# Optimization experiments

Hardware: AMD Instinct MI355X
Metric: run time of the kernel (lower is better)

The kernel has to match this reference:

```python
import jax, jax.numpy as jnp
import numpy as np

B, S, D, H = 2, 2048, 1024, 16
HD = D // H  # 64


def setup_inputs() -> dict:
    key = jax.random.key(0)
    k1, k2, k3, k4, k5, k6 = jax.random.split(key, 6)
    x = jax.random.normal(k1, (B, S, D), dtype=jnp.float32)
    # binary mask source (1.0 = masked-out position), multiplied by -1e9 inside
    mask = (jax.random.uniform(k2, (B, S, S), dtype=jnp.float32) < 0.1).astype(jnp.float32)
    lim = 1.0 / np.sqrt(D)
    Wqkv = jax.random.uniform(k3, (D, 3 * D), dtype=jnp.float32, minval=-lim, maxval=lim)
    bqkv = jax.random.uniform(k4, (3 * D,), dtype=jnp.float32, minval=-lim, maxval=lim)
    Wo = jax.random.uniform(k5, (D, D), dtype=jnp.float32, minval=-lim, maxval=lim)
    bo = jax.random.uniform(k6, (D,), dtype=jnp.float32, minval=-lim, maxval=lim)
    return {"x": x, "mask": mask, "Wqkv": Wqkv, "bqkv": bqkv, "Wo": Wo, "bo": bo}


def reference(x, mask, Wqkv, bqkv, Wo, bo):
    b, s, d = x.shape
    qkv = x @ Wqkv + bqkv                              # [B,S,3D]
    qkv = qkv.reshape(b, s, 3, H, HD).transpose(2, 0, 3, 1, 4)  # [3,B,H,S,HD]
    q, k, v = qkv[0], qkv[1], qkv[2]
    scale = 1.0 / jnp.sqrt(jnp.float32(HD))
    scores = jnp.einsum('bhqd,bhkd->bhqk', q, k) * scale
    scores = scores + mask[:, None, :, :] * (-1e9)     # broadcast over heads
    attn = jax.nn.softmax(scores, axis=-1)             # [B,H,S,S]
    values = jnp.einsum('bhqk,bhkd->bhqd', attn, v)    # [B,H,S,HD]
    # faithful to source: permute(1,0,2,3) then reshape(B,S,H*HD)
    values = values.transpose(1, 0, 2, 3).reshape(b, s, H * HD)
    return values @ Wo + bo
```

## Files before the change

kernel.cpp:

```cpp
#include <hip/hip_runtime.h>
#include <stdint.h>

#define BB 2
#define SS 2048
#define DD 1024
#define HH 16
#define HD 64
#define BH 32
#define BS 4096

typedef short bf16x8 __attribute__((ext_vector_type(8)));
typedef float f32x4 __attribute__((ext_vector_type(4)));

static __device__ __forceinline__ unsigned short f2bf(float f) {
    union { float f; unsigned int u; } x;
    x.f = f;
    unsigned int u = x.u;
    unsigned int r = u + 0x7FFFu + ((u >> 16) & 1u);
    return (unsigned short)(r >> 16);
}

static __device__ __forceinline__ void gld16(unsigned short* lds, const unsigned short* g) {
    __builtin_amdgcn_global_load_lds(
        (const __attribute__((address_space(1))) unsigned int*)g,
        (__attribute__((address_space(3))) unsigned int*)lds,
        16, 0, 0);
}

__global__ __launch_bounds__(256) void prep(
    const float* __restrict__ x, unsigned short* __restrict__ xb,
    const float* __restrict__ Wqkv, unsigned short* __restrict__ WqkvT,
    const float* __restrict__ Wo, unsigned short* __restrict__ WoT,
    const float* __restrict__ mask, unsigned int* __restrict__ mbitsT) {
    __shared__ float tile[32][33];
    int bid = blockIdx.x;
    int tid = threadIdx.x;
    if (bid < 4096) {
        int i = (bid * 256 + tid) * 4;
        float4 v = *(const float4*)(x + i);
        ushort4 o;
        o.x = f2bf(v.x); o.y = f2bf(v.y); o.z = f2bf(v.z); o.w = f2bf(v.w);
        *(ushort4*)(xb + i) = o;
    } else if (bid < 8192) {
        const float* W;
        unsigned short* WT;
        int N, t;
        if (bid < 7168) { W = Wqkv; WT = WqkvT; N = 3072; t = bid - 4096; }
        else            { W = Wo;   WT = WoT;   N = 1024; t = bid - 7168; }
        const int K = 1024;
        int nx = N >> 5;
        int n0 = (t % nx) * 32, k0 = (t / nx) * 32;
        int tx = tid & 31, ty = tid >> 5;
#pragma unroll
        for (int i = 0; i < 4; i++)
            tile[ty + i * 8][tx] = W[(size_t)(k0 + ty + i * 8) * N + n0 + tx];
        __syncthreads();
#pragma unroll
        for (int i = 0; i < 4; i++)
            WT[(size_t)(n0 + ty + i * 8) * K + k0 + tx] = f2bf(tile[tx][ty + i * 8]);
    } else {
        size_t i = (size_t)(bid - 8192) * 256 + tid;
        float v = mask[i];
        unsigned long long bal = __ballot(v != 0.0f);
        int lane = tid & 63;
        int kw = (int)((i & 2047) >> 5);
        int sq = (int)((i >> 11) & 2047);
        int b = (int)(i >> 22);
        if (lane == 0)
            mbitsT[((size_t)b * 64 + kw) * 2048 + sq] = (unsigned int)bal;
        else if (lane == 32)
            mbitsT[((size_t)b * 64 + kw) * 2048 + sq] = (unsigned int)(bal >> 32);
    }
}

__global__ __launch_bounds__(256) void qkv_gemm(
    const unsigned short* __restrict__ xb,
    const unsigned short* __restrict__ WqkvT,
    const float* __restrict__ bqkv,
    unsigned short* __restrict__ q_ws,
    unsigned short* __restrict__ k_ws,
    unsigned short* __restrict__ vB) {
    __shared__ unsigned short ldsA[4096], ldsB[4096];
    int gx = blockIdx.x;
    int tid = threadIdx.x;
    int m0 = (gx / 24) * 128, n0 = (gx % 24) * 128;
    int w = tid >> 6, lane = tid & 63, quad = lane >> 4, l15 = lane & 15;

    int r = tid >> 2, p = tid & 3;
    int c = (p - (r >> 1)) & 3;
    const unsigned short* gA0 = xb + (size_t)(m0 + r) * 1024 + c * 8;
    const unsigned short* gA1 = gA0 + (size_t)64 * 1024;
    const unsigned short* gB0 = WqkvT + (size_t)(n0 + r) * 1024 + c * 8;
    const unsigned short* gB1 = gB0 + (size_t)64 * 1024;
    unsigned short* lA0 = ldsA + w * 512;
    unsigned short* lA1 = ldsA + 2048 + w * 512;
    unsigned short* lB0 = ldsB + w * 512;
    unsigned short* lB1 = ldsB + 2048 + w * 512;

    int wm = w >> 1, wn = w & 1;
    int posq = ((quad + (l15 >> 1)) & 3) * 8;
    int aoff = (wm * 64 + l15) * 32 + posq;
    int boff = (wn * 64 + l15) * 32 + posq;

    f32x4 acc[4][4] = {};
    for (int k0 = 0; k0 < 1024; k0 += 32) {
        __syncthreads();
        gld16(lA0, gA0 + k0);
        gld16(lA1, gA1 + k0);
        gld16(lB0, gB0 + k0);
        gld16(lB1, gB1 + k0);
        __syncthreads();
        bf16x8 af[4], bfr[4];
#pragma unroll
        for (int i = 0; i < 4; i++) {
            af[i]  = *(const bf16x8*)(ldsA + aoff + i * 512);
            bfr[i] = *(const bf16x8*)(ldsB + boff + i * 512);
        }
#pragma unroll
        for (int i = 0; i < 4; i++)
#pragma unroll
            for (int j = 0; j < 4; j++)
                acc[i][j] = __builtin_amdgcn_mfma_f32_16x16x32_bf16(af[i], bfr[j], acc[i][j], 0, 0, 0);
    }

    int t = n0 >> 10;
    int ncol0 = n0 + wn * 64;
    int hh = (ncol0 >> 6) & 15;
    int Rb = m0 + wm * 64 + quad * 4;

    if (t == 2) {
        int rowbase = m0 + wm * 64;
        int b = rowbase >> 11;
        int kt = (rowbase >> 6) & 31;
        int bh = b * 16 + hh;
#pragma unroll
        for (int j = 0; j < 4; j++) {
            int hd = j * 16 + l15;
            float bias = bqkv[ncol0 + hd];
#pragma unroll
            for (int i = 0; i < 4; i++) {
                unsigned short* dst = vB +
                    (((((size_t)bh * 32 + kt) * 2 + (i >> 1)) * 4 + quad) * 64 + hd) * 8 + (i & 1) * 4;
                ushort4 pk;
                pk.x = f2bf(acc[i][j][0] + bias);
                pk.y = f2bf(acc[i][j][1] + bias);
                pk.z = f2bf(acc[i][j][2] + bias);
                pk.w = f2bf(acc[i][j][3] + bias);
                *(ushort4*)dst = pk;
            }
        }
    } else {
        unsigned short* dst = (t == 0) ? q_ws : k_ws;
#pragma unroll
        for (int j = 0; j < 4; j++) {
            int hd = j * 16 + l15;
            float bias = bqkv[ncol0 + hd];
#pragma unroll
            for (int i = 0; i < 4; i++) {
                int row = Rb + i * 16;
                int b = row >> 11, s = row & 2047;
                int bh = b * 16 + hh;
#pragma unroll
                for (int rr = 0; rr < 4; rr++)
                    dst[((size_t)(bh * 2048 + s + rr)) * 64 + hd] = f2bf(acc[i][j][rr] + bias);
            }
        }
    }
}

__global__ __launch_bounds__(256) void out_gemm(
    const unsigned short* __restrict__ Amat,
    const unsigned short* __restrict__ WoT,
    const float* __restrict__ bo,
    float* __restrict__ out) {
    __shared__ unsigned short ldsA[4096], ldsB[2048];
    int gx = blockIdx.x;
    int m0 = (gx / 16) * 128, n0 = (gx % 16) * 64;
    int tid = threadIdx.x;
    int w = tid >> 6, lane = tid & 63, quad = lane >> 4, l15 = lane & 15;

    int r = tid >> 2, p = tid & 3;
    int c = (p - (r >> 1)) & 3;
    const unsigned short* gA0 = Amat + (size_t)(m0 + r) * 1024 + c * 8;
    const unsigned short* gA1 = gA0 + (size_t)64 * 1024;
    const unsigned short* gB0 = WoT + (size_t)(n0 + r) * 1024 + c * 8;
    unsigned short* lA0 = ldsA + w * 512;
    unsigned short* lA1 = ldsA + 2048 + w * 512;
    unsigned short* lB0 = ldsB + w * 512;

    int wm = w >> 1, wn = w & 1;
    int posq = ((quad + (l15 >> 1)) & 3) * 8;
    int aoff = (wm * 64 + l15) * 32 + posq;
    int boff = (wn * 32 + l15) * 32 + posq;

    f32x4 acc[4][2] = {};
    for (int k0 = 0; k0 < 1024; k0 += 32) {
        __syncthreads();
        gld16(lA0, gA0 + k0);
        gld16(lA1, gA1 + k0);
        gld16(lB0, gB0 + k0);
        __syncthreads();
        bf16x8 af[4], bfr[2];
#pragma unroll
        for (int i = 0; i < 4; i++) af[i] = *(const bf16x8*)(ldsA + aoff + i * 512);
#pragma unroll
        for (int j = 0; j < 2; j++) bfr[j] = *(const bf16x8*)(ldsB + boff + j * 512);
#pragma unroll
        for (int i = 0; i < 4; i++)
#pragma unroll
            for (int j = 0; j < 2; j++)
                acc[i][j] = __builtin_amdgcn_mfma_f32_16x16x32_bf16(af[i], bfr[j], acc[i][j], 0, 0, 0);
    }
    int ncol0 = n0 + wn * 32;
    int Rb = m0 + wm * 64 + quad * 4;
#pragma unroll
    for (int j = 0; j < 2; j++) {
        int col = ncol0 + j * 16 + l15;
        float bias = bo[col];
#pragma unroll
        for (int i = 0; i < 4; i++) {
            int row = Rb + i * 16;
#pragma unroll
            for (int rr = 0; rr < 4; rr++)
                out[(size_t)(row + rr) * 1024 + col] = acc[i][j][rr] + bias;
        }
    }
}

__global__ __launch_bounds__(256) void attn(
    const unsigned short* __restrict__ q_ws,
    const unsigned short* __restrict__ k_ws,
    const unsigned short* __restrict__ vB,
    const unsigned int* __restrict__ mbitsT,
    unsigned short* __restrict__ o_ws) {
    __shared__ unsigned short ldsK[4096];
    __shared__ unsigned short ldsV[4096];

    int tid = threadIdx.x;
    int w = tid >> 6, lane = tid & 63, quad = lane >> 4, l15 = lane & 15;
    int bx = blockIdx.x;
    int bh = bx >> 5, qt = bx & 31;
    int b = bh >> 4, h = bh & 15;

    int q = qt * 64 + w * 16 + l15;
    const unsigned short* qptr = q_ws + ((size_t)(bh * 2048 + q)) * 64 + quad * 8;
    bf16x8 qf0 = *(const bf16x8*)(qptr);
    bf16x8 qf1 = *(const bf16x8*)(qptr + 32);

    const float c2 = 0.125f * 1.44269504089f;
    const float Cs = c2 * 8388608.0f;
    const float Ds = (127.0f - 16.0f) * 8388608.0f;

    const unsigned int* mb = mbitsT + (size_t)b * 64 * 2048 + q;
    const unsigned short* kbase = k_ws + (size_t)bh * 2048 * 64;
    const unsigned short* vbb = vB + (size_t)bh * 32 * 4096;

    int srow = (lane >> 3);
    int spos = lane & 7;
    unsigned short* dK0 = ldsK + w * 1024 + lane * 8;
    unsigned short* dK1 = dK0 + 512;
    unsigned short* dV0 = ldsV + w * 1024 + lane * 8;
    unsigned short* dV1 = dV0 + 512;
    int r0 = w * 16 + srow;
    int r1 = r0 + 8;
    int g0 = spos ^ (r0 & 7);
    int g1 = spos ^ (r1 & 7);

    f32x4 oacc[4] = {};
    f32x4 lacc = {};
    bf16x8 onesA;
#pragma unroll
    for (int j = 0; j < 8; j++) onesA[j] = (short)0x3F80;

    int sw = (l15 & 7);
    int q4 = quad * 4;
    for (int kt = 0; kt < 32; kt++) {
        __syncthreads();
        gld16(dK0, kbase + ((size_t)(kt * 64 + r0)) * 64 + g0 * 8);
        gld16(dK1, kbase + ((size_t)(kt * 64 + r1)) * 64 + g1 * 8);
        {
            const unsigned short* vsrc = vbb + (size_t)kt * 4096 + w * 1024 + lane * 8;
            gld16(dV0, vsrc);
            gld16(dV1, vsrc + 512);
        }
        __syncthreads();

        f32x4 sacc[4];
#pragma unroll
        for (int nt = 0; nt < 4; nt++) {
            const unsigned short* kr = ldsK + (nt * 16 + l15) * 64;
            bf16x8 kf0, kf1;
            __builtin_memcpy(&kf0, kr + (quad ^ sw) * 8, 16);
            __builtin_memcpy(&kf1, kr + ((quad + 4) ^ sw) * 8, 16);
            f32x4 z = {};
            z = __builtin_amdgcn_mfma_f32_16x16x32_bf16(kf0, qf0, z, 0, 0, 0);
            z = __builtin_amdgcn_mfma_f32_16x16x32_bf16(kf1, qf1, z, 0, 0, 0);
            sacc[nt] = z;
        }
        unsigned int w0 = mb[(size_t)(2 * kt) * 2048];
        unsigned int w1 = mb[(size_t)(2 * kt + 1) * 2048];
        unsigned int s0 = w0 >> q4;
        unsigned int s1 = w1 >> q4;
        unsigned int dw[4][2];
#pragma unroll
        for (int nt = 0; nt < 4; nt++) {
            unsigned int sel = (nt & 2) ? s1 : s0;
            unsigned int u[4];
#pragma unroll
            for (int rr = 0; rr < 4; rr++) {
                float y = __builtin_fmaf(sacc[nt][rr], Cs, Ds);
                if ((sel >> ((nt & 1) * 16 + rr)) & 1u) y = 0.f;
                u[rr] = (unsigned int)(int)y;
            }
            dw[nt][0] = __builtin_amdgcn_perm(u[1], u[0], 0x07060302u);
            dw[nt][1] = __builtin_amdgcn_perm(u[3], u[2], 0x07060302u);
        }
#pragma unroll
        for (int ks2 = 0; ks2 < 2; ks2++) {
            union { bf16x8 v; unsigned int d[4]; } bfr;
            bfr.d[0] = dw[2 * ks2][0];
            bfr.d[1] = dw[2 * ks2][1];
            bfr.d[2] = dw[2 * ks2 + 1][0];
            bfr.d[3] = dw[2 * ks2 + 1][1];
#pragma unroll
            for (int nb = 0; nb < 4; nb++) {
                bf16x8 vf;
                __builtin_memcpy(&vf, ldsV + ((ks2 * 4 + quad) * 64 + nb * 16 + l15) * 8, 16);
                oacc[nb] = __builtin_amdgcn_mfma_f32_16x16x32_bf16(vf, bfr.v, oacc[nb], 0, 0, 0);
            }
            lacc = __builtin_amdgcn_mfma_f32_16x16x32_bf16(onesA, bfr.v, lacc, 0, 0, 0);
        }
    }

    float linv = 1.0f / lacc[0];
    unsigned short* base = o_ws + ((size_t)((h * 2 + b) * 2048 + q)) * 64;
#pragma unroll
    for (int nb = 0; nb < 4; nb++) {
        ushort4 pk;
        pk.x = f2bf(oacc[nb][0] * linv);
        pk.y = f2bf(oacc[nb][1] * linv);
        pk.z = f2bf(oacc[nb][2] * linv);
        pk.w = f2bf(oacc[nb][3] * linv);
        *(ushort4*)(base + nb * 16 + quad * 4) = pk;
    }
}


extern "C" void kernel_launch(void* const* d_in, const int* in_sizes, int n_in,
                              void* d_out, int out_size, void* d_ws, size_t ws_size,
                              hipStream_t stream) {
    const float* x    = (const float*)d_in[0];
    const float* mask = (const float*)d_in[1];
    const float* Wqkv = (const float*)d_in[2];
    const float* bqkv = (const float*)d_in[3];
    const float* Wo   = (const float*)d_in[4];
    const float* bo   = (const float*)d_in[5];
    float* out = (float*)d_out;

    char* ws = (char*)d_ws;
    unsigned short* xb    = (unsigned short*)(ws);
    unsigned short* WqkvT = (unsigned short*)(ws + ((size_t)8 << 20));
    unsigned short* WoT   = (unsigned short*)(ws + ((size_t)14 << 20));
    unsigned short* q_ws  = (unsigned short*)(ws + ((size_t)16 << 20));
    unsigned short* k_ws  = (unsigned short*)(ws + ((size_t)24 << 20));
    unsigned short* vB    = (unsigned short*)(ws + ((size_t)32 << 20));
    unsigned short* o_ws  = (unsigned short*)(ws + ((size_t)40 << 20));
    unsigned int*   mbits = (unsigned int*)(ws + ((size_t)48 << 20));

    prep<<<8192 + 32768, 256, 0, stream>>>(x, xb, Wqkv, WqkvT, Wo, WoT, mask, mbits);
    qkv_gemm<<<768, 256, 0, stream>>>(xb, WqkvT, bqkv, q_ws, k_ws, vB);
    attn<<<1024, 256, 0, stream>>>(q_ws, k_ws, vB, mbits, o_ws);
    out_gemm<<<512, 256, 0, stream>>>(o_ws, WoT, bo, out);
}
```

Measured before the change: 231.4 us.

## Double-buffer K/V tiles and mask words in attention, remap block order

The attention loop now uses two LDS buffers for K and V. The next tile's global-to-LDS loads and mask-word loads are issued before computing on the current tile, which replaces the two barriers per iteration with one. The goal is to hide global load latency behind the MFMA work. Block indices are also permuted so that consecutive workgroups land on different (b,h) groups, which may improve cache and XCD locality. LDS use doubles to 32KB per block, which could lower occupancy.

```diff
diff --git a/kernel.cpp b/kernel.cpp
--- a/kernel.cpp
+++ b/kernel.cpp
@@ -233,12 +233,13 @@
     const unsigned short* __restrict__ vB,
     const unsigned int* __restrict__ mbitsT,
     unsigned short* __restrict__ o_ws) {
-    __shared__ unsigned short ldsK[4096];
-    __shared__ unsigned short ldsV[4096];
+    __shared__ unsigned short ldsK[8192];
+    __shared__ unsigned short ldsV[8192];
 
     int tid = threadIdx.x;
     int w = tid >> 6, lane = tid & 63, quad = lane >> 4, l15 = lane & 15;
-    int bx = blockIdx.x;
+    int bxr = blockIdx.x;
+    int bx = ((bxr & 7) << 7) | (bxr >> 3);
     int bh = bx >> 5, qt = bx & 31;
     int b = bh >> 4, h = bh & 15;
 
@@ -258,13 +259,14 @@
     int srow = (lane >> 3);
     int spos = lane & 7;
     unsigned short* dK0 = ldsK + w * 1024 + lane * 8;
-    unsigned short* dK1 = dK0 + 512;
     unsigned short* dV0 = ldsV + w * 1024 + lane * 8;
-    unsigned short* dV1 = dV0 + 512;
     int r0 = w * 16 + srow;
     int r1 = r0 + 8;
     int g0 = spos ^ (r0 & 7);
     int g1 = spos ^ (r1 & 7);
+    const unsigned short* kS0 = kbase + (size_t)r0 * 64 + g0 * 8;
+    const unsigned short* kS1 = kbase + (size_t)r1 * 64 + g1 * 8;
+    const unsigned short* vS  = vbb + (size_t)w * 1024 + lane * 8;
 
     f32x4 oacc[4] = {};
     f32x4 lacc = {};
@@ -274,21 +276,39 @@
 
     int sw = (l15 & 7);
     int q4 = quad * 4;
+
+    gld16(dK0, kS0);
+    gld16(dK0 + 512, kS1);
+    gld16(dV0, vS);
+    gld16(dV0 + 512, vS + 512);
+    unsigned int mw0 = mb[0];
+    unsigned int mw1 = mb[2048];
+    __syncthreads();
+
     for (int kt = 0; kt < 32; kt++) {
-        __syncthreads();
-        gld16(dK0, kbase + ((size_t)(kt * 64 + r0)) * 64 + g0 * 8);
-        gld16(dK1, kbase + ((size_t)(kt * 64 + r1)) * 64 + g1 * 8);
-        {
-            const unsigned short* vsrc = vbb + (size_t)kt * 4096 + w * 1024 + lane * 8;
-            gld16(dV0, vsrc);
-            gld16(dV1, vsrc + 512);
-        }
-        __syncthreads();
+        int co = (kt & 1) << 12;
+
+        unsigned int nw0 = 0, nw1 = 0;
+        if (kt < 31) {
+            int so = co ^ 4096;
+            const unsigned short* kn = kS0 + (size_t)(kt + 1) * 4096;
+            const unsigned short* kn1 = kS1 + (size_t)(kt + 1) * 4096;
+            const unsigned short* vn = vS + (size_t)(kt + 1) * 4096;
+            gld16(dK0 + so, kn);
+            gld16(dK0 + so + 512, kn1);
+            gld16(dV0 + so, vn);
+            gld16(dV0 + so + 512, vn + 512);
+            nw0 = mb[(size_t)(2 * kt + 2) * 2048];
+            nw1 = mb[(size_t)(2 * kt + 3) * 2048];
+        }
+
+        const unsigned short* Kc = ldsK + co;
+        const unsigned short* Vc = ldsV + co;
 
         f32x4 sacc[4];
 #pragma unroll
         for (int nt = 0; nt < 4; nt++) {
-            const unsigned short* kr = ldsK + (nt * 16 + l15) * 64;
+            const unsigned short* kr = Kc + (nt * 16 + l15) * 64;
             bf16x8 kf0, kf1;
             __builtin_memcpy(&kf0, kr + (quad ^ sw) * 8, 16);
             __builtin_memcpy(&kf1, kr + ((quad + 4) ^ sw) * 8, 16);
@@ -297,10 +317,8 @@
             z = __builtin_amdgcn_mfma_f32_16x16x32_bf16(kf1, qf1, z, 0, 0, 0);
             sacc[nt] = z;
         }
-        unsigned int w0 = mb[(size_t)(2 * kt) * 2048];
-        unsigned int w1 = mb[(size_t)(2 * kt + 1) * 2048];
-        unsigned int s0 = w0 >> q4;
-        unsigned int s1 = w1 >> q4;
+        unsigned int s0 = mw0 >> q4;
+        unsigned int s1 = mw1 >> q4;
         unsigned int dw[4][2];
 #pragma unroll
         for (int nt = 0; nt < 4; nt++) {
@@ -325,11 +343,15 @@
 #pragma unroll
             for (int nb = 0; nb < 4; nb++) {
                 bf16x8 vf;
-                __builtin_memcpy(&vf, ldsV + ((ks2 * 4 + quad) * 64 + nb * 16 + l15) * 8, 16);
+                __builtin_memcpy(&vf, Vc + ((ks2 * 4 + quad) * 64 + nb * 16 + l15) * 8, 16);
                 oacc[nb] = __builtin_amdgcn_mfma_f32_16x16x32_bf16(vf, bfr.v, oacc[nb], 0, 0, 0);
             }
             lacc = __builtin_amdgcn_mfma_f32_16x16x32_bf16(onesA, bfr.v, lacc, 0, 0, 0);
         }
+
+        __syncthreads();
+        mw0 = nw0;
+        mw1 = nw1;
     }
 
     float linv = 1.0f / lacc[0];
```

New measurement: 234.7 us. Within noise of the previous version (+1.5%).

## Double-buffer K/V tiles in attention, prefetch mask, remap blocks, set wave priority

Applied to the files above, without the earlier changes.

The attention kernel now uses two LDS buffers for K and V. It issues the global-to-LDS loads for the next key tile, and the next mask words, before computing on the current tile, which cuts one barrier per iteration and overlaps load latency with MFMA work. The block index is also permuted so that neighbouring workgroups handle different heads, and s_setprio raises wave priority around the MFMA sections. The cost is double the LDS footprint, which may lower occupancy. Correctness now relies on the single trailing barrier ordering buffer reuse.

```diff
diff --git a/kernel.cpp b/kernel.cpp
--- a/kernel.cpp
+++ b/kernel.cpp
@@ -233,12 +233,13 @@
     const unsigned short* __restrict__ vB,
     const unsigned int* __restrict__ mbitsT,
     unsigned short* __restrict__ o_ws) {
-    __shared__ unsigned short ldsK[4096];
-    __shared__ unsigned short ldsV[4096];
+    __shared__ unsigned short ldsK[8192];
+    __shared__ unsigned short ldsV[8192];
 
     int tid = threadIdx.x;
     int w = tid >> 6, lane = tid & 63, quad = lane >> 4, l15 = lane & 15;
-    int bx = blockIdx.x;
+    int bxr = blockIdx.x;
+    int bx = ((bxr & 7) << 7) | (bxr >> 3);
     int bh = bx >> 5, qt = bx & 31;
     int b = bh >> 4, h = bh & 15;
 
@@ -258,13 +259,15 @@
     int srow = (lane >> 3);
     int spos = lane & 7;
     unsigned short* dK0 = ldsK + w * 1024 + lane * 8;
-    unsigned short* dK1 = dK0 + 512;
     unsigned short* dV0 = ldsV + w * 1024 + lane * 8;
-    unsigned short* dV1 = dV0 + 512;
     int r0 = w * 16 + srow;
     int r1 = r0 + 8;
     int g0 = spos ^ (r0 & 7);
     int g1 = spos ^ (r1 & 7);
+    const unsigned short* kS0n = kbase + (size_t)r0 * 64 + g0 * 8;
+    const unsigned short* kS1n = kbase + (size_t)r1 * 64 + g1 * 8;
+    const unsigned short* vSn  = vbb + (size_t)w * 1024 + lane * 8;
+    const unsigned int* mbn = mb;
 
     f32x4 oacc[4] = {};
     f32x4 lacc = {};
@@ -274,63 +277,89 @@
 
     int sw = (l15 & 7);
     int q4 = quad * 4;
-    for (int kt = 0; kt < 32; kt++) {
-        __syncthreads();
-        gld16(dK0, kbase + ((size_t)(kt * 64 + r0)) * 64 + g0 * 8);
-        gld16(dK1, kbase + ((size_t)(kt * 64 + r1)) * 64 + g1 * 8);
-        {
-            const unsigned short* vsrc = vbb + (size_t)kt * 4096 + w * 1024 + lane * 8;
-            gld16(dV0, vsrc);
-            gld16(dV1, vsrc + 512);
-        }
-        __syncthreads();
-
-        f32x4 sacc[4];
-#pragma unroll
-        for (int nt = 0; nt < 4; nt++) {
-            const unsigned short* kr = ldsK + (nt * 16 + l15) * 64;
-            bf16x8 kf0, kf1;
-            __builtin_memcpy(&kf0, kr + (quad ^ sw) * 8, 16);
-            __builtin_memcpy(&kf1, kr + ((quad + 4) ^ sw) * 8, 16);
-            f32x4 z = {};
-            z = __builtin_amdgcn_mfma_f32_16x16x32_bf16(kf0, qf0, z, 0, 0, 0);
-            z = __builtin_amdgcn_mfma_f32_16x16x32_bf16(kf1, qf1, z, 0, 0, 0);
-            sacc[nt] = z;
-        }
-        unsigned int w0 = mb[(size_t)(2 * kt) * 2048];
-        unsigned int w1 = mb[(size_t)(2 * kt + 1) * 2048];
-        unsigned int s0 = w0 >> q4;
-        unsigned int s1 = w1 >> q4;
-        unsigned int dw[4][2];
-#pragma unroll
-        for (int nt = 0; nt < 4; nt++) {
-            unsigned int sel = (nt & 2) ? s1 : s0;
-            unsigned int u[4];
-#pragma unroll
-            for (int rr = 0; rr < 4; rr++) {
-                float y = __builtin_fmaf(sacc[nt][rr], Cs, Ds);
-                if ((sel >> ((nt & 1) * 16 + rr)) & 1u) y = 0.f;
-                u[rr] = (unsigned int)(int)y;
-            }
-            dw[nt][0] = __builtin_amdgcn_perm(u[1], u[0], 0x07060302u);
-            dw[nt][1] = __builtin_amdgcn_perm(u[3], u[2], 0x07060302u);
-        }
-#pragma unroll
-        for (int ks2 = 0; ks2 < 2; ks2++) {
-            union { bf16x8 v; unsigned int d[4]; } bfr;
-            bfr.d[0] = dw[2 * ks2][0];
-            bfr.d[1] = dw[2 * ks2][1];
-            bfr.d[2] = dw[2 * ks2 + 1][0];
-            bfr.d[3] = dw[2 * ks2 + 1][1];
-#pragma unroll
-            for (int nb = 0; nb < 4; nb++) {
-                bf16x8 vf;
-                __builtin_memcpy(&vf, ldsV + ((ks2 * 4 + quad) * 64 + nb * 16 + l15) * 8, 16);
-                oacc[nb] = __builtin_amdgcn_mfma_f32_16x16x32_bf16(vf, bfr.v, oacc[nb], 0, 0, 0);
-            }
-            lacc = __builtin_amdgcn_mfma_f32_16x16x32_bf16(onesA, bfr.v, lacc, 0, 0, 0);
-        }
-    }
+
+    gld16(dK0, kS0n);
+    gld16(dK0 + 512, kS1n);
+    gld16(dV0, vSn);
+    gld16(dV0 + 512, vSn + 512);
+    kS0n += 4096; kS1n += 4096; vSn += 4096;
+    unsigned int mw0 = mbn[0];
+    unsigned int mw1 = mbn[2048];
+    mbn += 4096;
+    __syncthreads();
+
+    unsigned int nw0, nw1;
+
+#define ATTN_BODY(KT, CO)                                                          \
+    {                                                                              \
+        nw0 = 0; nw1 = 0;                                                          \
+        if ((KT) < 31) {                 \
+            gld16(dK0 + ((CO) ^ 4096), kS0n);                                      \
+            gld16(dK0 + ((CO) ^ 4096) + 512, kS1n);                                \
+            gld16(dV0 + ((CO) ^ 4096), vSn);                                       \
+            gld16(dV0 + ((CO) ^ 4096) + 512, vSn + 512);                           \
+            kS0n += 4096; kS1n += 4096; vSn += 4096;                               \
+            nw0 = mbn[0]; nw1 = mbn[2048]; mbn += 4096;                            \
+        }                                                                          \
+        f32x4 sacc[4];                                                             \
+        __builtin_amdgcn_s_setprio(1);                                             \
+        _Pragma("unroll")                                                          \
+        for (int nt = 0; nt < 4; nt++) {                                           \
+            const unsigned short* kr = ldsK + (CO) + (nt * 16 + l15) * 64;         \
+            bf16x8 kf0, kf1;                                                       \
+            __builtin_memcpy(&kf0, kr + (quad ^ sw) * 8, 16);                      \
+            __builtin_memcpy(&kf1, kr + ((quad + 4) ^ sw) * 8, 16);                \
+            f32x4 z = {};                                                          \
+            z = __builtin_amdgcn_mfma_f32_16x16x32_bf16(kf0, qf0, z, 0, 0, 0);     \
+            z = __builtin_amdgcn_mfma_f32_16x16x32_bf16(kf1, qf1, z, 0, 0, 0);     \
+            sacc[nt] = z;                                                          \
+        }                                                                          \
+        __builtin_amdgcn_s_setprio(0);                                             \
+        unsigned int s0 = mw0 >> q4;                                               \
+        unsigned int s1 = mw1 >> q4;                                               \
+        unsigned int dw[4][2];                                                     \
+        _Pragma("unroll")                                                          \
+        for (int nt = 0; nt < 4; nt++) {                                           \
+            unsigned int sel = (nt & 2) ? s1 : s0;                                 \
+            unsigned int u[4];                                                     \
+            _Pragma("unroll")                                                      \
+            for (int rr = 0; rr < 4; rr++) {                                       \
+                float y = __builtin_fmaf(sacc[nt][rr], Cs, Ds);                    \
+                if ((sel >> ((nt & 1) * 16 + rr)) & 1u) y = 0.f;                   \
+                u[rr] = (unsigned int)(int)y;                                      \
+            }                                                                      \
+            dw[nt][0] = __builtin_amdgcn_perm(u[1], u[0], 0x07060302u);            \
+            dw[nt][1] = __builtin_amdgcn_perm(u[3], u[2], 0x07060302u);            \
+        }                                                                          \
+        __builtin_amdgcn_s_setprio(1);                                             \
+        _Pragma("unroll")                                                          \
+        for (int ks2 = 0; ks2 < 2; ks2++) {                                        \
+            union { bf16x8 v; unsigned int d[4]; } bfr;                            \
+            bfr.d[0] = dw[2 * ks2][0];                                             \
+            bfr.d[1] = dw[2 * ks2][1];                                             \
+            bfr.d[2] = dw[2 * ks2 + 1][0];                                         \
+            bfr.d[3] = dw[2 * ks2 + 1][1];                                         \
+            _Pragma("unroll")                                                      \
+            for (int nb = 0; nb < 4; nb++) {                                       \
+                bf16x8 vf;                                                         \
+                __builtin_memcpy(&vf,                                              \
+                    ldsV + (CO) + ((ks2 * 4 + quad) * 64 + nb * 16 + l15) * 8, 16);\
+                oacc[nb] = __builtin_amdgcn_mfma_f32_16x16x32_bf16(vf, bfr.v,      \
+                                                                   oacc[nb], 0, 0, 0); \
+            }                                                                      \
+            lacc = __builtin_amdgcn_mfma_f32_16x16x32_bf16(onesA, bfr.v, lacc,     \
+                                                           0, 0, 0);               \
+        }                                                                          \
+        __builtin_amdgcn_s_setprio(0);                                             \
+        __syncthreads();               \
+        mw0 = nw0; mw1 = nw1;                                                      \
+    }
+
+    for (int kt = 0; kt < 32; kt += 2) {
+        ATTN_BODY(kt, 0);
+        ATTN_BODY(kt + 1, 4096);
+    }
+#undef ATTN_BODY
 
     float linv = 1.0f / lacc[0];
     unsigned short* base = o_ws + ((size_t)((h * 2 + b) * 2048 + q)) * 64;
```

Result: no change. 232.3 us (+0.4%).
